# Performance work log

Measured on AMD Instinct MI355X. Metric: run time of the kernel, lower is better.

Reference implementation:

```python
import jax, jax.numpy as jnp
import numpy as np

SNAPPING_GAIN = 30.0


def setup_inputs() -> dict:
    key = jax.random.key(0)
    k1, k2 = jax.random.split(key)
    latent_coeffs = jax.random.normal(k1, (16, 2048, 1024), dtype=jnp.float32)
    # NMF basis is non-negative; 1024 atoms of dim 900 (30x30 ARC grids)
    basis_vectors = jax.random.uniform(k2, (1024, 900), dtype=jnp.float32)
    return {"latent_coeffs": latent_coeffs, "basis_vectors": basis_vectors}


def reference(latent_coeffs, basis_vectors):
    # [B, K, C] -> sharpened softmax over codes
    probs = jax.nn.softmax(latent_coeffs * SNAPPING_GAIN, axis=-1)
    indices = jnp.argmax(probs, axis=-1)                        # [B, K] int
    one_hot = jax.nn.one_hot(indices, probs.shape[-1], dtype=probs.dtype)
    # straight-through: value == one_hot, gradient flows through probs
    one_hot_st = probs + jax.lax.stop_gradient(one_hot - probs)
    # [B,K,C] @ [C,D] -> [B,K,D] (effectively a row-gather of the basis)
    quantized = jnp.einsum('bkc,cd->bkd', one_hot_st, basis_vectors)
    return quantized, indices
```

## Files before the change

### kernel.cpp

```cpp
#include <hip/hip_runtime.h>


#define C_DIM 1024
#define D_DIM 900

typedef float vfloat4 __attribute__((ext_vector_type(4)));

__global__ __launch_bounds__(256) void basisvq_kernel(
    const float* __restrict__ latent,
    const float* __restrict__ basis,
    float* __restrict__ out_q,
    float* __restrict__ out_idx,
    int rows)
{
    const int lane = threadIdx.x & 63;
    const int wid  = threadIdx.x >> 6;
    const int row  = blockIdx.x * 4 + wid;
    if (row >= rows) return;

    const vfloat4* lrow = reinterpret_cast<const vfloat4*>(latent + (size_t)row * C_DIM);
    vfloat4 v0 = __builtin_nontemporal_load(&lrow[lane]);
    vfloat4 v1 = __builtin_nontemporal_load(&lrow[lane + 64]);
    vfloat4 v2 = __builtin_nontemporal_load(&lrow[lane + 128]);
    vfloat4 v3 = __builtin_nontemporal_load(&lrow[lane + 192]);

    float m = v0[0];
    int   mi = lane * 4;
    #pragma unroll
    for (int e = 1; e < 4; ++e)
        if (v0[e] > m) { m = v0[e]; mi = lane * 4 + e; }
    #pragma unroll
    for (int e = 0; e < 4; ++e)
        if (v1[e] > m) { m = v1[e]; mi = (64 + lane) * 4 + e; }
    #pragma unroll
    for (int e = 0; e < 4; ++e)
        if (v2[e] > m) { m = v2[e]; mi = (128 + lane) * 4 + e; }
    #pragma unroll
    for (int e = 0; e < 4; ++e)
        if (v3[e] > m) { m = v3[e]; mi = (192 + lane) * 4 + e; }

    #pragma unroll
    for (int off = 32; off > 0; off >>= 1) {
        float om = __shfl_xor(m, off, 64);
        int   oi = __shfl_xor(mi, off, 64);
        if (om > m || (om == m && oi < mi)) { m = om; mi = oi; }
    }
    const int idx = mi;

    if (lane == 0) out_idx[row] = (float)idx;

    const vfloat4* b4 = reinterpret_cast<const vfloat4*>(basis + (size_t)idx * D_DIM);
    vfloat4*       o4 = reinterpret_cast<vfloat4*>(out_q + (size_t)row * D_DIM);
    #pragma unroll
    for (int j = 0; j < 4; ++j) {
        int t = 64 * j + lane;
        if (t < 225) {
            vfloat4 bv = b4[t];
            o4[t] = bv;
        }
    }
}

extern "C" void kernel_launch(void* const* d_in, const int* in_sizes, int n_in,
                              void* d_out, int out_size, void* d_ws, size_t ws_size,
                              hipStream_t stream) {
    const float* latent = (const float*)d_in[0];
    const float* basis  = (const float*)d_in[1];
    (void)n_in; (void)d_ws; (void)ws_size; (void)out_size;

    const int rows = in_sizes[0] / C_DIM;
    float* out_q   = (float*)d_out;
    float* out_idx = (float*)d_out + (size_t)rows * D_DIM;

    const int blocks = (rows + 3) / 4;
    basisvq_kernel<<<blocks, 256, 0, stream>>>(latent, basis, out_q, out_idx, rows);
}
```

Baseline: 53.83 us.

## Split into argmax pass and per-code scatter kernel using shared-memory basis rows

Splits the fused kernel in two. The first kernel only computes per-row argmax indices. The second kernel assigns two codes to each block, loads their basis rows into shared memory, scans all indices to build a worklist of matching rows, and writes those rows with nontemporal stores. This aims to replace scattered global basis reads with shared-memory reads, but it adds a second launch and makes every block rescan the full 32K index array. The worklist is capped at 1024 entries, so heavily used codes would be silently dropped.

```diff
diff --git a/kernel.cpp b/kernel.cpp
--- a/kernel.cpp
+++ b/kernel.cpp
@@ -3,13 +3,13 @@
 
 #define C_DIM 1024
 #define D_DIM 900
+#define CPB   2
+#define WL_CAP 1024
 
 typedef float vfloat4 __attribute__((ext_vector_type(4)));
 
-__global__ __launch_bounds__(256) void basisvq_kernel(
+__global__ __launch_bounds__(256) void argmax_kernel(
     const float* __restrict__ latent,
-    const float* __restrict__ basis,
-    float* __restrict__ out_q,
     float* __restrict__ out_idx,
     int rows)
 {
@@ -45,18 +45,56 @@
         int   oi = __shfl_xor(mi, off, 64);
         if (om > m || (om == m && oi < mi)) { m = om; mi = oi; }
     }
-    const int idx = mi;
 
-    if (lane == 0) out_idx[row] = (float)idx;
+    if (lane == 0) out_idx[row] = (float)mi;
+}
 
-    const vfloat4* b4 = reinterpret_cast<const vfloat4*>(basis + (size_t)idx * D_DIM);
-    vfloat4*       o4 = reinterpret_cast<vfloat4*>(out_q + (size_t)row * D_DIM);
-    #pragma unroll
-    for (int j = 0; j < 4; ++j) {
-        int t = 64 * j + lane;
-        if (t < 225) {
-            vfloat4 bv = b4[t];
-            o4[t] = bv;
+__global__ __launch_bounds__(256) void scatter_kernel(
+    const float* __restrict__ basis,
+    const float* __restrict__ out_idx,
+    float* __restrict__ out_q,
+    int rows)
+{
+    __shared__ float bs[CPB * D_DIM];
+    __shared__ int   wl[WL_CAP];
+    __shared__ int   cnt;
+
+    const int tid   = threadIdx.x;
+    const int code0 = blockIdx.x * CPB;
+
+    if (tid == 0) cnt = 0;
+    for (int j = tid; j < CPB * D_DIM; j += 256)
+        bs[j] = basis[(size_t)code0 * D_DIM + j];
+    __syncthreads();
+
+    const float lo = (float)code0, hi = (float)(code0 + CPB);
+    const int n4 = rows >> 2;
+    const vfloat4* idx4 = reinterpret_cast<const vfloat4*>(out_idx);
+    for (int i = tid; i < n4; i += 256) {
+        vfloat4 f = idx4[i];
+        #pragma unroll
+        for (int e = 0; e < 4; ++e) {
+            if (f[e] >= lo && f[e] < hi) {
+                int lc = (int)f[e] - code0;
+                int p  = atomicAdd(&cnt, 1);
+                if (p < WL_CAP) wl[p] = ((i * 4 + e) << 1) | lc;
+            }
+        }
+    }
+    __syncthreads();
+
+    const int n    = cnt < WL_CAP ? cnt : WL_CAP;
+    const int lane = tid & 63;
+    const int wid  = tid >> 6;
+    for (int w = wid; w < n; w += 4) {
+        const int e   = wl[w];
+        const int row = e >> 1;
+        const vfloat4* s4 = reinterpret_cast<const vfloat4*>(&bs[(e & 1) * D_DIM]);
+        vfloat4*       o4 = reinterpret_cast<vfloat4*>(out_q + (size_t)row * D_DIM);
+        #pragma unroll
+        for (int j = 0; j < 4; ++j) {
+            int t = 64 * j + lane;
+            if (t < 225) __builtin_nontemporal_store(s4[t], &o4[t]);
         }
     }
 }
@@ -72,6 +110,6 @@
     float* out_q   = (float*)d_out;
     float* out_idx = (float*)d_out + (size_t)rows * D_DIM;
 
-    const int blocks = (rows + 3) / 4;
-    basisvq_kernel<<<blocks, 256, 0, stream>>>(latent, basis, out_q, out_idx, rows);
+    argmax_kernel<<<(rows + 3) / 4, 256, 0, stream>>>(latent, out_idx, rows);
+    scatter_kernel<<<(C_DIM + CPB - 1) / CPB, 256, 0, stream>>>(basis, out_idx, out_q, rows);
 }
```

Measured after the change: 65.66 us. 1.22x slower.
